# Kernel tuning notes

Hardware: AMD Instinct MI355X
Metric: run time of the kernel (lower is better)

The kernel has to match this reference:

```python
import jax, jax.numpy as jnp
import numpy as np
from jax import lax

HD = 64      # head_dim
PS = 2       # fine patch size
EPS = 1e-5   # batchnorm eps

def _conv(x, w, stride, pad, groups=1):
    return lax.conv_general_dilated(x, w, (stride, stride), ((pad, pad), (pad, pad)),
                                    feature_group_count=groups,
                                    dimension_numbers=('NCHW', 'OIHW', 'NCHW'))

def _conv_transpose(x, w, stride, pad):
    # torch ConvTranspose2d(in,out,k,stride,pad) with w [in,out,k,k]
    k = w.shape[-1]
    wt = jnp.flip(w, (2, 3)).transpose(1, 0, 2, 3)  # -> [out,in,k,k]
    e = k - 1 - pad
    return lax.conv_general_dilated(x, wt, (1, 1), ((e, e), (e, e)),
                                    lhs_dilation=(stride, stride),
                                    dimension_numbers=('NCHW', 'OIHW', 'NCHW'))

def _bn(x, g, b, m, v):
    inv = g / jnp.sqrt(v + EPS)
    return x * inv[None, :, None, None] + (b - m * inv)[None, :, None, None]

def setup_inputs() -> dict:
    key = jax.random.key(0)
    ks = jax.random.split(key, 12)
    B, C, H, W = 8, 256, 64, 64
    f = lambda k, sh, s=0.05: jax.random.normal(k, sh, jnp.float32) * s
    return {
        'x': jax.random.normal(ks[0], (B, C, H, W), jnp.float32),
        'down_w': f(ks[1], (C, C, 4, 4), 0.02), 'down_b': f(ks[2], (C,)),
        'up_w': f(ks[3], (C, C, 4, 4), 0.02), 'up_b': f(ks[4], (C,)),
        'wqkv_c': f(ks[5], (HD, 3 * HD)), 'bqkv_c': f(ks[6], (3 * HD,)),
        'wqkv_f': f(ks[7], (HD, 3 * HD)), 'bqkv_f': f(ks[8], (3 * HD,)),
        'dw_w': f(ks[9], (C, 1, 3, 3)),
        'bn1_g': jnp.ones((C,), jnp.float32), 'bn1_b': jnp.zeros((C,), jnp.float32),
        'bn1_m': jnp.zeros((C,), jnp.float32), 'bn1_v': jnp.ones((C,), jnp.float32),
        'pw_w': f(ks[10], (C, C, 1, 1)),
        'bn2_g': jnp.ones((C,), jnp.float32), 'bn2_b': jnp.zeros((C,), jnp.float32),
        'bn2_m': jnp.zeros((C,), jnp.float32), 'bn2_v': jnp.ones((C,), jnp.float32),
    }

def reference(x, down_w, down_b, up_w, up_b, wqkv_c, bqkv_c, wqkv_f, bqkv_f, dw_w,
              bn1_g, bn1_b, bn1_m, bn1_v, pw_w, bn2_g, bn2_b, bn2_m, bn2_v):
    B, C, H, W = x.shape
    nh = C // HD
    scale = HD ** -0.5

    # ---- CoarseSelfAttention: downsample -> per-head MHSA -> top-k -> upsample ----
    xd = _conv(x, down_w, 2, 1) + down_b[None, :, None, None]          # [B,C,H/2,W/2]
    h, w = H // 2, W // 2
    N = h * w
    tok = xd.reshape(B, nh, HD, N).transpose(0, 1, 3, 2)               # [B,nh,N,hd]
    q, k, v = jnp.split(tok @ wqkv_c + bqkv_c, 3, axis=-1)
    attn = jax.nn.softmax(jnp.einsum('bhnd,bhmd->bhnm', q, k) * scale, axis=-1)
    score = attn.sum(axis=-2)                                          # [B,nh,N]
    kf = max(1, N // 4)
    topk = lax.top_k(score, kf)[1]                                     # [B,nh,kf] int32
    out = jnp.einsum('bhnm,bhmd->bhnd', attn, v)
    out = out.transpose(0, 1, 3, 2).reshape(B, C, h, w)
    coarse = _conv_transpose(out, up_w, 2, 1) + up_b[None, :, None, None]  # [B,C,H,W]
    # F.interpolate to (H,W) is identity here: upsample output already matches x.

    # ---- TopkSelfAttention: gather top-k 2x2 patches, local MHSA, scatter back ----
    ph, pw = H // PS, W // PS
    xh = coarse.reshape(B, nh, HD, ph, PS, pw, PS)
    patches = xh.transpose(0, 1, 2, 3, 5, 4, 6).reshape(B, nh, HD, ph * pw, PS, PS)
    sel = jnp.take_along_axis(patches, topk[:, :, None, :, None, None], axis=3)  # [B,nh,hd,kf,PS,PS]
    tok_f = sel.reshape(B, nh, HD, kf, PS * PS).transpose(0, 1, 3, 4, 2).reshape(B, nh, kf * PS * PS, HD)
    qf, kfp, vf = jnp.split(tok_f @ wqkv_f + bqkv_f, 3, axis=-1)
    attn_f = jax.nn.softmax(jnp.einsum('bhnd,bhmd->bhnm', qf, kfp) * scale, axis=-1)
    out_f = jnp.einsum('bhnm,bhmd->bhnd', attn_f, vf)                  # [B,nh,kf*4,hd]
    out_p = out_f.reshape(B, nh, kf, PS * PS, HD).transpose(0, 1, 2, 4, 3).reshape(B, nh, kf, HD, PS, PS)
    bi = jnp.arange(B)[:, None, None]
    hi = jnp.arange(nh)[None, :, None]
    res = jnp.zeros_like(patches).at[bi, hi, :, topk].set(out_p)       # scatter (indices unique)
    region = res.reshape(B, nh, HD, ph, pw, PS, PS).transpose(0, 1, 2, 3, 5, 4, 6).reshape(B, C, H, W)

    # ---- residual + DWConv (depthwise->BN->ReLU6->pointwise->BN->ReLU6) ----
    y = coarse + region
    y = jnp.clip(_bn(_conv(y, dw_w, 1, 1, groups=C), bn1_g, bn1_b, bn1_m, bn1_v), 0.0, 6.0)
    y = jnp.clip(_bn(_conv(y, pw_w, 1, 0), bn2_g, bn2_b, bn2_m, bn2_v), 0.0, 6.0)
    return y
```

## Files before the change

kernel.cpp:

```cpp
#include <hip/hip_runtime.h>
#include <hip/hip_bf16.h>

typedef __hip_bfloat16 bf16;
typedef __bf16 bf16x8 __attribute__((ext_vector_type(8)));
typedef float f32x4 __attribute__((ext_vector_type(4)));
typedef unsigned int uintx4 __attribute__((ext_vector_type(4)));


#define OFF_XDHWC    0L
#define OFF_QH       2097152L
#define OFF_T1       0L
#define OFF_OUTC     8388608L
#define OFF_COARSE   10485760L
#define OFF_XHL      10485760L
#define OFF_PSCW     10485760L
#define OFF_SCORE    19398656L
#define OFF_TOPK     19431424L
#define OFF_DOWNW    19439616L
#define OFF_DOWNWL   19963904L
#define OFF_UPW4     20488192L
#define OFF_WQKVC    21536768L
#define OFF_BQKVC    21549056L
#define OFF_WQKVF    21549248L
#define OFF_BQKVF    21561536L
#define OFF_PWW      21561728L
#define OFF_DWW      21627264L
#define OFF_BN1S     21629568L
#define OFF_BN1T     21629824L
#define OFF_BN2S     21630080L
#define OFF_BN2T     21630336L
#define OFF_DOWNB    21630592L
#define OFF_UPB      21630848L
#define OFF_FLAG     21631104L
#define WS_FLOATS    21631360L

__device__ __forceinline__ float relu6(float v) { return v < 0.f ? 0.f : (v > 6.f ? 6.f : v); }

__device__ __forceinline__ float ldin(const void* p, long i, int flag) {
    return flag ? __bfloat162float(((const bf16*)p)[i]) : ((const float*)p)[i];
}

__device__ __forceinline__ unsigned short f2bf(float f) {
    unsigned int b = __float_as_uint(f);
    b += 0x7FFFu + ((b >> 16) & 1u);
    return (unsigned short)(b >> 16);
}

__global__ __launch_bounds__(256) void detect_kernel(const void* __restrict__ x, int* __restrict__ flag) {
    __shared__ int cnt[256];
    int tid = threadIdx.x;
    int c = 0;
    for (int i = tid; i < 4096; i += 256) {
        long idx = (long)i * 2047;
        float v = __bfloat162float(((const bf16*)x)[idx]);
        float a = fabsf(v);
        if (isfinite(v) && a > 1e-8f && a < 100.f) c++;
    }
    cnt[tid] = c; __syncthreads();
    for (int s = 128; s > 0; s >>= 1) { if (tid < s) cnt[tid] += cnt[tid + s]; __syncthreads(); }
    if (tid == 0 && cnt[0] >= 3686) *flag = 1;
}

__global__ __launch_bounds__(256) void cvt_kernel(const void* __restrict__ in, float* __restrict__ out,
                                                  int n, const int* __restrict__ flagp) {
    int flag = *flagp;
    int i = blockIdx.x * 256 + threadIdx.x;
    if (i < n) out[i] = ldin(in, i, flag);
}

__global__ __launch_bounds__(256) void cvt_bf16_kernel(const void* __restrict__ in, unsigned short* __restrict__ out,
                                                       int n, const int* __restrict__ flagp) {
    int flag = *flagp;
    int i = blockIdx.x * 256 + threadIdx.x;
    if (i < n) out[i] = f2bf(ldin(in, i, flag));
}

__global__ __launch_bounds__(256) void split_pack_kernel(const void* __restrict__ in, unsigned int* __restrict__ out,
                                                         int n, const int* __restrict__ flagp) {
    int flag = *flagp;
    int i = blockIdx.x * 256 + threadIdx.x;
    if (i < n) {
        float v = ldin(in, i, flag);
        unsigned short h = f2bf(v);
        float fh = __uint_as_float(((unsigned int)h) << 16);
        unsigned short l = f2bf(v - fh);
        out[i] = (unsigned int)h | ((unsigned int)l << 16);
    }
}

__global__ __launch_bounds__(256) void split_kernel(const void* __restrict__ in,
                                                    unsigned short* __restrict__ hi, unsigned short* __restrict__ lo,
                                                    int n, const int* __restrict__ flagp) {
    int flag = *flagp;
    int i = blockIdx.x * 256 + threadIdx.x;
    if (i < n) {
        float v = ldin(in, i, flag);
        unsigned short h = f2bf(v);
        float fh = __uint_as_float(((unsigned int)h) << 16);
        hi[i] = h;
        lo[i] = f2bf(v - fh);
    }
}

__global__ __launch_bounds__(256) void tqkv_kernel(const void* __restrict__ w, float* __restrict__ wt,
                                                   const int* __restrict__ flagp) {
    int flag = *flagp;
    int idx = blockIdx.x * 256 + threadIdx.x;
    if (idx >= 192 * 64) return;
    int j = idx >> 6, d = idx & 63;
    wt[idx] = ldin(w, d * 192 + j, flag);
}

__global__ __launch_bounds__(256) void prep_up_kernel(const void* __restrict__ w, unsigned short* __restrict__ W4,
                                                      const int* __restrict__ flagp) {
    int flag = *flagp;
    int idx = blockIdx.x * 256 + threadIdx.x;
    int cls = idx >> 18; int rem = idx & 262143;
    int co = rem >> 10; int q = rem & 1023;
    int ci = q >> 2; int j = q & 3;
    int pa = cls >> 1, pb = cls & 1;
    int jy = j >> 1, jx = j & 1;
    int ky = (pa == 0) ? (jy ? 3 : 1) : (jy ? 0 : 2);
    int kx = (pb == 0) ? (jx ? 3 : 1) : (jx ? 0 : 2);
    W4[idx] = f2bf(ldin(w, (((long)ci * 256 + co) * 4 + ky) * 4 + kx, flag));
}

__global__ void bn_prep_kernel(const void* __restrict__ g, const void* __restrict__ b,
                               const void* __restrict__ m, const void* __restrict__ v,
                               float* __restrict__ s, float* __restrict__ t,
                               const int* __restrict__ flagp) {
    int flag = *flagp;
    int c = threadIdx.x;
    float gv = ldin(g, c, flag), bv = ldin(b, c, flag);
    float mv = ldin(m, c, flag), vv = ldin(v, c, flag);
    float inv = gv / sqrtf(vv + 1e-5f);
    s[c] = inv; t[c] = bv - mv * inv;
}

__global__ __launch_bounds__(256) void gemm_mfma_x2(
    const unsigned int* __restrict__ XHL,
    const unsigned short* __restrict__ WH, const unsigned short* __restrict__ WL,
    float* __restrict__ C, const float* __restrict__ e0)
{
    __shared__ __align__(16) unsigned int Xs[40 * 68];
    __shared__ __align__(16) unsigned short Bh[64 * 72];
    __shared__ __align__(16) unsigned short Bl[64 * 72];
    int m0 = blockIdx.y * 128, n0 = blockIdx.x * 64;
    int tid = threadIdx.x;
    int w = tid >> 6, l = tid & 63, l15 = l & 15, q = l >> 4;

    int offA[11], ldsA[11];
    {
        int b = m0 >> 10;
        int iy0 = ((m0 >> 5) & 31) * 2 - 1;
        #pragma unroll
        for (int s = 0; s < 11; s++) {
            int u = s * 256 + tid;
            offA[s] = -1; ldsA[s] = -1;
            if (u < 2640) {
                int R = u / 66;
                int col = u - R * 66;
                int cl = R / 10;
                int rowl = R - cl * 10;
                ldsA[s] = R * 68 + col;
                int iy = iy0 + rowl, ix = col - 1;
                if ((unsigned)iy < 64u && (unsigned)ix < 64u)
                    offA[s] = ((b * 256 + cl) * 64 + iy) * 64 + ix;
            }
        }
    }
    unsigned int aR[11];
    uint4 bhR[2], blR[2];
    int bn = tid >> 2, bkc = (tid & 3) * 16;

    auto loadA = [&](int k0) {
        int cb = (k0 >> 4) * 4096;
        #pragma unroll
        for (int s = 0; s < 11; s++)
            aR[s] = (offA[s] >= 0) ? XHL[offA[s] + cb] : 0u;
    };
    auto storeA = [&]() {
        #pragma unroll
        for (int s = 0; s < 11; s++)
            if (ldsA[s] >= 0) Xs[ldsA[s]] = aR[s];
    };
    auto loadB = [&](int k0) {
        const unsigned short* ph = WH + (long)(n0 + bn) * 4096 + k0 + bkc;
        const unsigned short* pl = WL + (long)(n0 + bn) * 4096 + k0 + bkc;
        bhR[0] = *(const uint4*)(ph); bhR[1] = *(const uint4*)(ph + 8);
        blR[0] = *(const uint4*)(pl); blR[1] = *(const uint4*)(pl + 8);
    };
    auto storeB = [&]() {
        *(uint4*)(&Bh[bn * 72 + bkc]) = bhR[0]; *(uint4*)(&Bh[bn * 72 + bkc + 8]) = bhR[1];
        *(uint4*)(&Bl[bn * 72 + bkc]) = blR[0]; *(uint4*)(&Bl[bn * 72 + bkc + 8]) = blR[1];
    };

    f32x4 acc[2][4] = {};
    loadA(0); loadB(0);
    for (int k0 = 0; k0 < 4096; k0 += 64) {
        storeA(); storeB();
        __syncthreads();
        if (k0 + 64 < 4096) { loadA(k0 + 64); loadB(k0 + 64); }
        #pragma unroll
        for (int kk = 0; kk < 2; kk++) {
            bf16x8 bh4[4], bl4[4];
            #pragma unroll
            for (int j4 = 0; j4 < 4; j4++) {
                bh4[j4] = *(const bf16x8*)(&Bh[(j4 * 16 + l15) * 72 + kk * 32 + q * 8]);
                bl4[j4] = *(const bf16x8*)(&Bl[(j4 * 16 + l15) * 72 + kk * 32 + q * 8]);
            }
            int R0 = (kk * 2 + (q >> 1)) * 10 + 2 * w + 2 * (q & 1);
            #pragma unroll
            for (int ms = 0; ms < 2; ms++) {
                const unsigned int* rp = &Xs[R0 * 68 + 2 * (ms * 16 + l15)];
                uint2 p01 = *(const uint2*)(rp);
                uint2 p23 = *(const uint2*)(rp + 2);
                uint2 p45 = *(const uint2*)(rp + 68);
                uint2 p67 = *(const uint2*)(rp + 70);
                union { uintx4 u; bf16x8 v; } uh, ul;
                uh.u[0] = __builtin_amdgcn_perm(p01.y, p01.x, 0x05040100u);
                ul.u[0] = __builtin_amdgcn_perm(p01.y, p01.x, 0x07060302u);
                uh.u[1] = __builtin_amdgcn_perm(p23.y, p23.x, 0x05040100u);
                ul.u[1] = __builtin_amdgcn_perm(p23.y, p23.x, 0x07060302u);
                uh.u[2] = __builtin_amdgcn_perm(p45.y, p45.x, 0x05040100u);
                ul.u[2] = __builtin_amdgcn_perm(p45.y, p45.x, 0x07060302u);
                uh.u[3] = __builtin_amdgcn_perm(p67.y, p67.x, 0x05040100u);
                ul.u[3] = __builtin_amdgcn_perm(p67.y, p67.x, 0x07060302u);
                #pragma unroll
                for (int j4 = 0; j4 < 4; j4++) {
                    acc[ms][j4] = __builtin_amdgcn_mfma_f32_16x16x32_bf16(uh.v, bh4[j4], acc[ms][j4], 0, 0, 0);
                    acc[ms][j4] = __builtin_amdgcn_mfma_f32_16x16x32_bf16(uh.v, bl4[j4], acc[ms][j4], 0, 0, 0);
                    acc[ms][j4] = __builtin_amdgcn_mfma_f32_16x16x32_bf16(ul.v, bh4[j4], acc[ms][j4], 0, 0, 0);
                }
            }
        }
        __syncthreads();
    }
    #pragma unroll
    for (int ms = 0; ms < 2; ms++)
        #pragma unroll
        for (int j4 = 0; j4 < 4; j4++) {
            int n = n0 + j4 * 16 + l15;
            #pragma unroll
            for (int r = 0; r < 4; r++) {
                int m = m0 + w * 32 + ms * 16 + q * 4 + r;
                C[(long)m * 256 + n] = acc[ms][j4][r] + e0[n];
            }
        }
}

template<int EPI>
__global__ __launch_bounds__(256) void gemm_k(
    const float* __restrict__ A, const float* __restrict__ B, unsigned short* __restrict__ out,
    int K, int sAm, int sBn, const float* __restrict__ e0)
{
    __shared__ float As[16][68];
    __shared__ float Bs[16][68];
    int m0 = blockIdx.y * 64;
    int n0 = blockIdx.x * 64;
    int tid = threadIdx.x;
    int tx = tid & 15, ty = tid >> 4;
    int l4 = tid >> 2, kq = (tid & 3) * 4;
    float4 aR, bR;

    auto loadA = [&](int k0) { aR = *(const float4*)(A + (long)(m0 + l4) * sAm + (k0 + kq)); };
    auto loadB = [&](int k0) { bR = *(const float4*)(B + (long)(n0 + l4) * sBn + (k0 + kq)); };

    float acc[4][4] = {};
    loadA(0); loadB(0);
    for (int k0 = 0; k0 < K; k0 += 16) {
        As[kq + 0][l4] = aR.x; As[kq + 1][l4] = aR.y; As[kq + 2][l4] = aR.z; As[kq + 3][l4] = aR.w;
        Bs[kq + 0][l4] = bR.x; Bs[kq + 1][l4] = bR.y; Bs[kq + 2][l4] = bR.z; Bs[kq + 3][l4] = bR.w;
        __syncthreads();
        if (k0 + 16 < K) { loadA(k0 + 16); loadB(k0 + 16); }
        #pragma unroll
        for (int kk = 0; kk < 16; ++kk) {
            float4 av = *reinterpret_cast<const float4*>(&As[kk][ty * 4]);
            float4 bv = *reinterpret_cast<const float4*>(&Bs[kk][tx * 4]);
            float a[4] = {av.x, av.y, av.z, av.w};
            float b[4] = {bv.x, bv.y, bv.z, bv.w};
            #pragma unroll
            for (int i = 0; i < 4; i++)
                #pragma unroll
                for (int j = 0; j < 4; j++)
                    acc[i][j] += a[i] * b[j];
        }
        __syncthreads();
    }
    #pragma unroll
    for (int i = 0; i < 4; i++) {
        int m = m0 + ty * 4 + i;
        int bh, tok;
        if (EPI == 2) { int bi = m >> 12; int h = m & 3; tok = (m >> 2) & 1023; bh = bi * 4 + h; }
        else          { bh = m >> 10; tok = m & 1023; }
        #pragma unroll
        for (int j = 0; j < 4; j++) {
            int n = n0 + tx * 4 + j;
            float v = acc[i][j] + e0[n];
            if (n < 64) {
                v *= 0.125f;
                unsigned short hb = f2bf(v);
                float fh = __uint_as_float(((unsigned int)hb) << 16);
                unsigned short lb = f2bf(v - fh);
                long p = (((long)bh << 10) + tok) * 64 + n;
                out[p] = hb; out[p + 2097152] = lb;
            } else if (n < 128) {
                unsigned short hb = f2bf(v);
                float fh = __uint_as_float(((unsigned int)hb) << 16);
                unsigned short lb = f2bf(v - fh);
                long p = (((long)bh << 10) + tok) * 64 + (n - 64);
                out[p + 4194304] = hb; out[p + 6291456] = lb;
            } else {
                out[8388608 + (((long)bh << 6) + (n - 128)) * 1024 + tok] = f2bf(v);
            }
        }
    }
}

template<int EPI, int AMODE>
__global__ __launch_bounds__(256) void gemm_mfma(
    const float* __restrict__ A, const unsigned short* __restrict__ Bb, float* __restrict__ C,
    int K, long sAz, long sBz, int sAk, int sBn,
    const float* __restrict__ e0, const float* __restrict__ e1,
    void* __restrict__ ob, const int* __restrict__ flagp)
{
    __shared__ __align__(16) unsigned short Asb[64 * 40];
    __shared__ __align__(16) unsigned short Bsb[64 * 40];
    int z = blockIdx.z;
    if (AMODE == 0) A += (long)z * sAz;
    Bb += (long)z * sBz;
    int m0 = blockIdx.y * 64, n0 = blockIdx.x * 64;
    int tid = threadIdx.x;
    int w = tid >> 6, l = tid & 63;
    int l15 = l & 15, q = l >> 4;
    float aR[8];
    uint4 bR;

    auto loadA = [&](int k0) {
        if (AMODE == 0) {
            #pragma unroll
            for (int i = 0; i < 8; i++) {
                int idx = i * 256 + tid;
                int ml = idx & 63, kl = idx >> 6;
                aR[i] = A[(long)(k0 + kl) * sAk + (m0 + ml)];
            }
        } else {
            #pragma unroll
            for (int i = 0; i < 8; i++) {
                int idx = i * 256 + tid;
                int kl = idx & 31, ml = idx >> 5;
                int m = m0 + ml, k = k0 + kl;
                int b = m >> 10, y = (m >> 5) & 31, x2 = m & 31;
                int ci = k >> 2, j = k & 3;
                int pa = z >> 1, pb = z & 1;
                int jy = j >> 1, jx = j & 1;
                int dy = (pa == 0) ? (jy ? -1 : 0) : (jy ? 1 : 0);
                int dx = (pb == 0) ? (jx ? -1 : 0) : (jx ? 1 : 0);
                int yy = y + dy, xx = x2 + dx;
                float val = 0.f;
                if ((unsigned)yy < 32u && (unsigned)xx < 32u)
                    val = A[(((long)b * 4 + (ci >> 6)) * 1024 + yy * 32 + xx) * 64 + (ci & 63)];
                aR[i] = val;
            }
        }
    };
    auto storeA = [&]() {
        #pragma unroll
        for (int i = 0; i < 8; i++) {
            int idx = i * 256 + tid;
            int ml, kl;
            if (AMODE == 0) { ml = idx & 63; kl = idx >> 6; }
            else            { kl = idx & 31; ml = idx >> 5; }
            Asb[ml * 40 + kl] = f2bf(aR[i]);
        }
    };
    int bn = tid >> 2, bk = (tid & 3) * 8;
    auto loadB = [&](int k0) {
        bR = *(const uint4*)(Bb + (long)(n0 + bn) * sBn + (k0 + bk));
    };

    f32x4 acc[4] = {};
    loadA(0); loadB(0);
    for (int k0 = 0; k0 < K; k0 += 32) {
        storeA();
        *(uint4*)(&Bsb[bn * 40 + bk]) = bR;
        __syncthreads();
        if (k0 + 32 < K) { loadA(k0 + 32); loadB(k0 + 32); }
        bf16x8 af = *(const bf16x8*)(&Asb[(w * 16 + l15) * 40 + q * 8]);
        #pragma unroll
        for (int j4 = 0; j4 < 4; j4++) {
            bf16x8 bf = *(const bf16x8*)(&Bsb[(j4 * 16 + l15) * 40 + q * 8]);
            acc[j4] = __builtin_amdgcn_mfma_f32_16x16x32_bf16(af, bf, acc[j4], 0, 0, 0);
        }
        __syncthreads();
    }
    int oflag = (EPI == 5) ? *flagp : 0;
    #pragma unroll
    for (int j4 = 0; j4 < 4; j4++) {
        int n = n0 + j4 * 16 + l15;
        #pragma unroll
        for (int r = 0; r < 4; r++) {
            int m = m0 + w * 16 + q * 4 + r;
            float v = acc[j4][r];
            if (EPI == 4) {
                v += e0[n];
                int pa = z >> 1, pb = z & 1;
                int bi = m >> 10, y = (m >> 5) & 31, x2 = m & 31;
                C[(((long)bi * 256 + n) * 64 + (2 * y + pa)) * 64 + (2 * x2 + pb)] = v;
            } else {
                v = relu6(v * e0[n] + e1[n]);
                long oidx = (long)z * 1048576 + (long)n * 4096 + m;
                if (oflag) ((bf16*)ob)[oidx] = __float2bfloat16(v);
                else       ((float*)ob)[oidx] = v;
            }
        }
    }
}

template<bool SCORE>
__global__ __launch_bounds__(256) void attn_mfma(
    const unsigned short* __restrict__ P0,
    float* __restrict__ O, float* __restrict__ PSCW)
{
    const unsigned short* QH = P0;
    const unsigned short* QL = P0 + 2097152;
    const unsigned short* KH = P0 + 4194304;
    const unsigned short* KL = P0 + 6291456;
    const unsigned short* VT = P0 + 8388608;
    __shared__ __align__(16) unsigned short Khs[64 * 72];
    __shared__ __align__(16) unsigned short Kls[64 * 72];
    __shared__ __align__(16) unsigned short Vs[64 * 72];
    __shared__ __align__(16) unsigned short Ps[4][16 * 72];
    int bh = blockIdx.y, rt = blockIdx.x;
    int tid = threadIdx.x;
    int w = tid >> 6, l = tid & 63, l15 = l & 15, q = l >> 4;

    long qoff = (((long)bh << 10) + rt * 64 + w * 16 + l15) * 64 + q * 8;
    bf16x8 afh[2], afl[2];
    afh[0] = *(const bf16x8*)(QH + qoff);
    afh[1] = *(const bf16x8*)(QH + qoff + 32);
    afl[0] = *(const bf16x8*)(QL + qoff);
    afl[1] = *(const bf16x8*)(QL + qoff + 32);

    float mr[4], lr[4];
    #pragma unroll
    for (int r = 0; r < 4; r++) { mr[r] = -1e30f; lr[r] = 0.f; }
    f32x4 o[4] = {};

    auto stageK = [&](int t) {
        #pragma unroll
        for (int i = 0; i < 2; i++) {
            int u = tid + i * 256;
            int tok = u >> 3, dp = (u & 7) * 8;
            long g = (((long)bh << 10) + t * 64 + tok) * 64 + dp;
            *(uint4*)(Khs + tok * 72 + dp) = *(const uint4*)(KH + g);
            *(uint4*)(Kls + tok * 72 + dp) = *(const uint4*)(KL + g);
        }
    };
    auto stageV = [&](int t) {
        #pragma unroll
        for (int i = 0; i < 2; i++) {
            int u = tid + i * 256;
            int d = u >> 3, k0 = (u & 7) * 8;
            long g = (((long)bh << 6) + d) * 1024 + t * 64 + k0;
            *(uint4*)(Vs + d * 72 + k0) = *(const uint4*)(VT + g);
        }
    };
    auto computeS = [&](f32x4* s) {
        #pragma unroll
        for (int kk = 0; kk < 2; kk++)
            #pragma unroll
            for (int j4 = 0; j4 < 4; j4++) {
                bf16x8 kh8 = *(const bf16x8*)(&Khs[(j4 * 16 + l15) * 72 + kk * 32 + q * 8]);
                bf16x8 kl8 = *(const bf16x8*)(&Kls[(j4 * 16 + l15) * 72 + kk * 32 + q * 8]);
                s[j4] = __builtin_amdgcn_mfma_f32_16x16x32_bf16(afh[kk], kh8, s[j4], 0, 0, 0);
                s[j4] = __builtin_amdgcn_mfma_f32_16x16x32_bf16(afh[kk], kl8, s[j4], 0, 0, 0);
                s[j4] = __builtin_amdgcn_mfma_f32_16x16x32_bf16(afl[kk], kh8, s[j4], 0, 0, 0);
            }
    };
    auto pv = [&]() {
        #pragma unroll
        for (int kk = 0; kk < 2; kk++) {
            bf16x8 ap = *(const bf16x8*)(&Ps[w][l15 * 72 + kk * 32 + q * 8]);
            #pragma unroll
            for (int j4 = 0; j4 < 4; j4++) {
                bf16x8 bv = *(const bf16x8*)(&Vs[(j4 * 16 + l15) * 72 + kk * 32 + q * 8]);
                o[j4] = __builtin_amdgcn_mfma_f32_16x16x32_bf16(ap, bv, o[j4], 0, 0, 0);
            }
        }
    };

    if (SCORE) {
        for (int t = 0; t < 16; ++t) {
            __syncthreads();
            stageK(t);
            __syncthreads();
            f32x4 s[4] = {};
            computeS(s);
            #pragma unroll
            for (int r = 0; r < 4; r++) {
                float tm = fmaxf(fmaxf(s[0][r], s[1][r]), fmaxf(s[2][r], s[3][r]));
                #pragma unroll
                for (int off = 1; off < 16; off <<= 1) tm = fmaxf(tm, __shfl_xor(tm, off));
                float mn = fmaxf(mr[r], tm);
                float ss = __expf(s[0][r] - mn) + __expf(s[1][r] - mn)
                         + __expf(s[2][r] - mn) + __expf(s[3][r] - mn);
                #pragma unroll
                for (int off = 1; off < 16; off <<= 1) ss += __shfl_xor(ss, off);
                lr[r] = lr[r] * __expf(mr[r] - mn) + ss;
                mr[r] = mn;
            }
        }
        float linv[4];
        #pragma unroll
        for (int r = 0; r < 4; r++) linv[r] = 1.f / lr[r];
        for (int t = 0; t < 16; ++t) {
            __syncthreads();
            stageK(t); stageV(t);
            __syncthreads();
            f32x4 s[4] = {};
            computeS(s);
            float cs[4] = {0.f, 0.f, 0.f, 0.f};
            #pragma unroll
            for (int j4 = 0; j4 < 4; j4++)
                #pragma unroll
                for (int r = 0; r < 4; r++) {
                    float p = __expf(s[j4][r] - mr[r]) * linv[r];
                    cs[j4] += p;
                    Ps[w][(q * 4 + r) * 72 + j4 * 16 + l15] = f2bf(p);
                }
            #pragma unroll
            for (int j4 = 0; j4 < 4; j4++) {
                cs[j4] += __shfl_xor(cs[j4], 16);
                cs[j4] += __shfl_xor(cs[j4], 32);
            }
            if (q == 0) {
                long pb = (((long)(bh * 16 + rt) * 4 + w) << 10) + t * 64;
                #pragma unroll
                for (int j4 = 0; j4 < 4; j4++) PSCW[pb + j4 * 16 + l15] = cs[j4];
            }
            __syncthreads();
            pv();
        }
    } else {
        for (int t = 0; t < 16; ++t) {
            __syncthreads();
            stageK(t); stageV(t);
            __syncthreads();
            f32x4 s[4] = {};
            computeS(s);
            float corr[4];
            #pragma unroll
            for (int r = 0; r < 4; r++) {
                float tm = fmaxf(fmaxf(s[0][r], s[1][r]), fmaxf(s[2][r], s[3][r]));
                #pragma unroll
                for (int off = 1; off < 16; off <<= 1) tm = fmaxf(tm, __shfl_xor(tm, off));
                float mn = fmaxf(mr[r], tm);
                corr[r] = __expf(mr[r] - mn);
                mr[r] = mn;
            }
            float ssr[4] = {0.f, 0.f, 0.f, 0.f};
            #pragma unroll
            for (int j4 = 0; j4 < 4; j4++)
                #pragma unroll
                for (int r = 0; r < 4; r++) {
                    float p = __expf(s[j4][r] - mr[r]);
                    ssr[r] += p;
                    Ps[w][(q * 4 + r) * 72 + j4 * 16 + l15] = f2bf(p);
                }
            #pragma unroll
            for (int r = 0; r < 4; r++) {
                float ss = ssr[r];
                #pragma unroll
                for (int off = 1; off < 16; off <<= 1) ss += __shfl_xor(ss, off);
                lr[r] = lr[r] * corr[r] + ss;
            }
            #pragma unroll
            for (int j4 = 0; j4 < 4; j4++)
                #pragma unroll
                for (int r = 0; r < 4; r++) o[j4][r] *= corr[r];
            __syncthreads();
            pv();
        }
    }

    float fin[4];
    #pragma unroll
    for (int r = 0; r < 4; r++) fin[r] = SCORE ? 1.f : (1.f / lr[r]);
    long obase = (((long)bh << 10) + rt * 64 + w * 16 + q * 4) * 64;
    #pragma unroll
    for (int j4 = 0; j4 < 4; j4++)
        #pragma unroll
        for (int r = 0; r < 4; r++)
            O[obase + (long)r * 64 + j4 * 16 + l15] = o[j4][r] * fin[r];
}

__global__ __launch_bounds__(256) void score_reduce_kernel(const float* __restrict__ PSCW, float* __restrict__ score) {
    int idx = blockIdx.x * 256 + threadIdx.x;
    int bh = idx >> 10, c = idx & 1023;
    float s = 0.f;
    for (int rw = 0; rw < 64; rw++) s += PSCW[(((long)bh * 64 + rw) << 10) + c];
    score[idx] = s;
}

__global__ __launch_bounds__(256) void topk_kernel(const float* __restrict__ score, int* __restrict__ topk) {
    __shared__ float s[1024];
    int z = blockIdx.x; int tid = threadIdx.x;
    for (int i = tid; i < 1024; i += 256) {
        float v = score[z * 1024 + i];
        s[i] = (v == v) ? v : -INFINITY;
    }
    __syncthreads();
    for (int i = tid; i < 1024; i += 256) {
        float si = s[i]; int r = 0;
        for (int j = 0; j < 1024; j++) {
            float sj = s[j];
            r += (sj > si) || (sj == si && j < i);
        }
        if (r < 256) topk[z * 256 + r] = i;
    }
}

__global__ __launch_bounds__(256) void gather_tokf_kernel(const float* __restrict__ coarse,
                                                          const int* __restrict__ topk,
                                                          float* __restrict__ tokf) {
    long idx = (long)blockIdx.x * 256 + threadIdx.x;
    int d = (int)(idx & 63); int t = (int)((idx >> 6) & 3);
    int j = (int)((idx >> 8) & 255); int bh = (int)(idx >> 16);
    int p = topk[bh * 256 + j] & 1023;
    int py = p >> 5, px = p & 31;
    int dy = t >> 1, dx = t & 1;
    int b = bh >> 2, h = bh & 3;
    tokf[idx] = coarse[(((long)b * 256 + h * 64 + d) * 64 + (2 * py + dy)) * 64 + (2 * px + dx)];
}

__global__ __launch_bounds__(256) void scatter_add_kernel(float* __restrict__ coarse,
                                                          const int* __restrict__ topk,
                                                          const float* __restrict__ outf) {
    long idx = (long)blockIdx.x * 256 + threadIdx.x;
    int d = (int)(idx & 63); int t = (int)((idx >> 6) & 3);
    int j = (int)((idx >> 8) & 255); int bh = (int)(idx >> 16);
    int p = topk[bh * 256 + j] & 1023;
    int py = p >> 5, px = p & 31;
    int dy = t >> 1, dx = t & 1;
    int b = bh >> 2, h = bh & 3;
    coarse[(((long)b * 256 + h * 64 + d) * 64 + (2 * py + dy)) * 64 + (2 * px + dx)] += outf[idx];
}

__global__ __launch_bounds__(64) void dw_bn_relu6_kernel(const float* __restrict__ y, const float* __restrict__ w9,
                                                         const float* __restrict__ s1, const float* __restrict__ t1,
                                                         float* __restrict__ out) {
    int gid = blockIdx.x;
    int row = gid & 63; int bc = gid >> 6; int c = bc & 255;
    int x = threadIdx.x;
    const float* base = y + (long)bc * 4096;
    float acc = 0.f;
    #pragma unroll
    for (int ky = 0; ky < 3; ky++) {
        int yy = row + ky - 1;
        if (yy < 0 || yy >= 64) continue;
        #pragma unroll
        for (int kx = 0; kx < 3; kx++) {
            int xx = x + kx - 1;
            if (xx < 0 || xx >= 64) continue;
            acc += base[yy * 64 + xx] * w9[c * 9 + ky * 3 + kx];
        }
    }
    out[(long)gid * 64 + x] = relu6(acc * s1[c] + t1[c]);
}

extern "C" void kernel_launch(void* const* d_in, const int* in_sizes, int n_in,
                              void* d_out, int out_size, void* d_ws, size_t ws_size,
                              hipStream_t stream) {
    if (ws_size < (size_t)WS_FLOATS * 4) return;

    const void* x      = d_in[0];
    const void* down_w = d_in[1];
    const void* down_b = d_in[2];
    const void* up_w   = d_in[3];
    const void* up_b   = d_in[4];
    const void* wqkv_c = d_in[5];
    const void* bqkv_c = d_in[6];
    const void* wqkv_f = d_in[7];
    const void* bqkv_f = d_in[8];
    const void* dw_w   = d_in[9];
    const void* bn1_g  = d_in[10];
    const void* bn1_b  = d_in[11];
    const void* bn1_m  = d_in[12];
    const void* bn1_v  = d_in[13];
    const void* pw_w   = d_in[14];
    const void* bn2_g  = d_in[15];
    const void* bn2_b  = d_in[16];
    const void* bn2_m  = d_in[17];
    const void* bn2_v  = d_in[18];

    float* ws = (float*)d_ws;
    int* flagp = (int*)(ws + OFF_FLAG);
    dim3 blk(256);

    hipMemsetAsync(flagp, 0, sizeof(int), stream);
    detect_kernel<<<1, blk, 0, stream>>>(x, flagp);

    split_pack_kernel<<<32768, blk, 0, stream>>>(x, (unsigned int*)(ws + OFF_XHL), 8388608, flagp);
    split_kernel<<<4096, blk, 0, stream>>>(down_w, (unsigned short*)(ws + OFF_DOWNW),
                                           (unsigned short*)(ws + OFF_DOWNWL), 1048576, flagp);
    cvt_kernel<<<1, blk, 0, stream>>>(down_b, ws + OFF_DOWNB, 256, flagp);
    cvt_kernel<<<1, blk, 0, stream>>>(up_b, ws + OFF_UPB, 256, flagp);
    cvt_kernel<<<1, blk, 0, stream>>>(bqkv_c, ws + OFF_BQKVC, 192, flagp);
    cvt_kernel<<<1, blk, 0, stream>>>(bqkv_f, ws + OFF_BQKVF, 192, flagp);
    cvt_bf16_kernel<<<256, blk, 0, stream>>>(pw_w, (unsigned short*)(ws + OFF_PWW), 65536, flagp);
    cvt_kernel<<<9, blk, 0, stream>>>(dw_w, ws + OFF_DWW, 2304, flagp);
    tqkv_kernel<<<48, blk, 0, stream>>>(wqkv_c, ws + OFF_WQKVC, flagp);
    tqkv_kernel<<<48, blk, 0, stream>>>(wqkv_f, ws + OFF_WQKVF, flagp);
    prep_up_kernel<<<4096, blk, 0, stream>>>(up_w, (unsigned short*)(ws + OFF_UPW4), flagp);
    bn_prep_kernel<<<1, blk, 0, stream>>>(bn1_g, bn1_b, bn1_m, bn1_v, ws + OFF_BN1S, ws + OFF_BN1T, flagp);
    bn_prep_kernel<<<1, blk, 0, stream>>>(bn2_g, bn2_b, bn2_m, bn2_v, ws + OFF_BN2S, ws + OFF_BN2T, flagp);

    gemm_mfma_x2<<<dim3(4, 64, 1), blk, 0, stream>>>((const unsigned int*)(ws + OFF_XHL),
        (const unsigned short*)(ws + OFF_DOWNW), (const unsigned short*)(ws + OFF_DOWNWL),
        ws + OFF_XDHWC, ws + OFF_DOWNB);

    gemm_k<2><<<dim3(3, 512, 1), blk, 0, stream>>>(ws + OFF_XDHWC, ws + OFF_WQKVC,
        (unsigned short*)(ws + OFF_QH), 64, 64, 64, ws + OFF_BQKVC);

    attn_mfma<true><<<dim3(16, 32), blk, 0, stream>>>((const unsigned short*)(ws + OFF_QH),
        ws + OFF_OUTC, ws + OFF_PSCW);
    score_reduce_kernel<<<128, blk, 0, stream>>>(ws + OFF_PSCW, ws + OFF_SCORE);
    topk_kernel<<<32, blk, 0, stream>>>(ws + OFF_SCORE, (int*)(ws + OFF_TOPK));

    gemm_mfma<4, 2><<<dim3(4, 128, 4), blk, 0, stream>>>(ws + OFF_OUTC, (unsigned short*)(ws + OFF_UPW4),
        ws + OFF_COARSE, 1024, 0, 262144, 0, 1024, ws + OFF_UPB, nullptr, nullptr, flagp);

    gather_tokf_kernel<<<8192, blk, 0, stream>>>(ws + OFF_COARSE, (const int*)(ws + OFF_TOPK), ws + OFF_XDHWC);
    gemm_k<3><<<dim3(3, 512, 1), blk, 0, stream>>>(ws + OFF_XDHWC, ws + OFF_WQKVF,
        (unsigned short*)(ws + OFF_QH), 64, 64, 64, ws + OFF_BQKVF);
    attn_mfma<false><<<dim3(16, 32), blk, 0, stream>>>((const unsigned short*)(ws + OFF_QH),
        ws + OFF_OUTC, nullptr);
    scatter_add_kernel<<<8192, blk, 0, stream>>>(ws + OFF_COARSE, (const int*)(ws + OFF_TOPK), ws + OFF_OUTC);

    dw_bn_relu6_kernel<<<131072, dim3(64), 0, stream>>>(ws + OFF_COARSE, ws + OFF_DWW,
        ws + OFF_BN1S, ws + OFF_BN1T, ws + OFF_T1);

    gemm_mfma<5, 0><<<dim3(4, 64, 8), blk, 0, stream>>>(ws + OFF_T1, (unsigned short*)(ws + OFF_PWW),
        nullptr, 256, 1048576, 0, 4096, 256, ws + OFF_BN2S, ws + OFF_BN2T, d_out, flagp);
}
```

Before: 850.7 us.

## Split-K and smaller M tile for downsample conv GEMM, sum partials in QKV GEMM

The downsample conv GEMM now uses 64-row M tiles and splits K into two halves across blockIdx.z. This raises the grid from 256 to 1024 blocks to improve occupancy across the CUs. The two partial results go to separate buffers, and the following QKV GEMM adds them while loading its A operand, so no separate reduction pass is needed. The cost is extra global traffic for the second partial buffer and less reuse of each B tile within a block.

After: 839.5 us. No clear change (-1.3%).

```diff
diff --git a/kernel.cpp b/kernel.cpp
--- a/kernel.cpp
+++ b/kernel.cpp
@@ -140,28 +140,29 @@
 __global__ __launch_bounds__(256) void gemm_mfma_x2(
     const unsigned int* __restrict__ XHL,
     const unsigned short* __restrict__ WH, const unsigned short* __restrict__ WL,
-    float* __restrict__ C, const float* __restrict__ e0)
+    float* __restrict__ C0, float* __restrict__ C1, const float* __restrict__ e0)
 {
-    __shared__ __align__(16) unsigned int Xs[40 * 68];
+    __shared__ __align__(16) unsigned int Xs[24 * 68];
     __shared__ __align__(16) unsigned short Bh[64 * 72];
     __shared__ __align__(16) unsigned short Bl[64 * 72];
-    int m0 = blockIdx.y * 128, n0 = blockIdx.x * 64;
+    int m0 = blockIdx.y * 64, n0 = blockIdx.x * 64;
+    int kz = blockIdx.z * 2048;
     int tid = threadIdx.x;
     int w = tid >> 6, l = tid & 63, l15 = l & 15, q = l >> 4;
 
-    int offA[11], ldsA[11];
+    int offA[7], ldsA[7];
     {
         int b = m0 >> 10;
         int iy0 = ((m0 >> 5) & 31) * 2 - 1;
         #pragma unroll
-        for (int s = 0; s < 11; s++) {
+        for (int s = 0; s < 7; s++) {
             int u = s * 256 + tid;
             offA[s] = -1; ldsA[s] = -1;
-            if (u < 2640) {
+            if (u < 1584) {
                 int R = u / 66;
                 int col = u - R * 66;
-                int cl = R / 10;
-                int rowl = R - cl * 10;
+                int cl = R / 6;
+                int rowl = R - cl * 6;
                 ldsA[s] = R * 68 + col;
                 int iy = iy0 + rowl, ix = col - 1;
                 if ((unsigned)iy < 64u && (unsigned)ix < 64u)
@@ -169,24 +170,24 @@
             }
         }
     }
-    unsigned int aR[11];
+    unsigned int aR[7];
     uint4 bhR[2], blR[2];
     int bn = tid >> 2, bkc = (tid & 3) * 16;
 
     auto loadA = [&](int k0) {
-        int cb = (k0 >> 4) * 4096;
-        #pragma unroll
-        for (int s = 0; s < 11; s++)
+        int cb = (((kz + k0) >> 4)) * 4096;
+        #pragma unroll
+        for (int s = 0; s < 7; s++)
             aR[s] = (offA[s] >= 0) ? XHL[offA[s] + cb] : 0u;
     };
     auto storeA = [&]() {
         #pragma unroll
-        for (int s = 0; s < 11; s++)
+        for (int s = 0; s < 7; s++)
             if (ldsA[s] >= 0) Xs[ldsA[s]] = aR[s];
     };
     auto loadB = [&](int k0) {
-        const unsigned short* ph = WH + (long)(n0 + bn) * 4096 + k0 + bkc;
-        const unsigned short* pl = WL + (long)(n0 + bn) * 4096 + k0 + bkc;
+        const unsigned short* ph = WH + (long)(n0 + bn) * 4096 + kz + k0 + bkc;
+        const unsigned short* pl = WL + (long)(n0 + bn) * 4096 + kz + k0 + bkc;
         bhR[0] = *(const uint4*)(ph); bhR[1] = *(const uint4*)(ph + 8);
         blR[0] = *(const uint4*)(pl); blR[1] = *(const uint4*)(pl + 8);
     };
@@ -195,12 +196,12 @@
         *(uint4*)(&Bl[bn * 72 + bkc]) = blR[0]; *(uint4*)(&Bl[bn * 72 + bkc + 8]) = blR[1];
     };
 
-    f32x4 acc[2][4] = {};
+    f32x4 acc[4] = {};
     loadA(0); loadB(0);
-    for (int k0 = 0; k0 < 4096; k0 += 64) {
+    for (int k0 = 0; k0 < 2048; k0 += 64) {
         storeA(); storeB();
         __syncthreads();
-        if (k0 + 64 < 4096) { loadA(k0 + 64); loadB(k0 + 64); }
+        if (k0 + 64 < 2048) { loadA(k0 + 64); loadB(k0 + 64); }
         #pragma unroll
         for (int kk = 0; kk < 2; kk++) {
             bf16x8 bh4[4], bl4[4];
@@ -209,50 +210,47 @@
                 bh4[j4] = *(const bf16x8*)(&Bh[(j4 * 16 + l15) * 72 + kk * 32 + q * 8]);
                 bl4[j4] = *(const bf16x8*)(&Bl[(j4 * 16 + l15) * 72 + kk * 32 + q * 8]);
             }
-            int R0 = (kk * 2 + (q >> 1)) * 10 + 2 * w + 2 * (q & 1);
-            #pragma unroll
-            for (int ms = 0; ms < 2; ms++) {
-                const unsigned int* rp = &Xs[R0 * 68 + 2 * (ms * 16 + l15)];
-                uint2 p01 = *(const uint2*)(rp);
-                uint2 p23 = *(const uint2*)(rp + 2);
-                uint2 p45 = *(const uint2*)(rp + 68);
-                uint2 p67 = *(const uint2*)(rp + 70);
-                union { uintx4 u; bf16x8 v; } uh, ul;
-                uh.u[0] = __builtin_amdgcn_perm(p01.y, p01.x, 0x05040100u);
-                ul.u[0] = __builtin_amdgcn_perm(p01.y, p01.x, 0x07060302u);
-                uh.u[1] = __builtin_amdgcn_perm(p23.y, p23.x, 0x05040100u);
-                ul.u[1] = __builtin_amdgcn_perm(p23.y, p23.x, 0x07060302u);
-                uh.u[2] = __builtin_amdgcn_perm(p45.y, p45.x, 0x05040100u);
-                ul.u[2] = __builtin_amdgcn_perm(p45.y, p45.x, 0x07060302u);
-                uh.u[3] = __builtin_amdgcn_perm(p67.y, p67.x, 0x05040100u);
-                ul.u[3] = __builtin_amdgcn_perm(p67.y, p67.x, 0x07060302u);
-                #pragma unroll
-                for (int j4 = 0; j4 < 4; j4++) {
-                    acc[ms][j4] = __builtin_amdgcn_mfma_f32_16x16x32_bf16(uh.v, bh4[j4], acc[ms][j4], 0, 0, 0);
-                    acc[ms][j4] = __builtin_amdgcn_mfma_f32_16x16x32_bf16(uh.v, bl4[j4], acc[ms][j4], 0, 0, 0);
-                    acc[ms][j4] = __builtin_amdgcn_mfma_f32_16x16x32_bf16(ul.v, bh4[j4], acc[ms][j4], 0, 0, 0);
-                }
+            int R0 = (2 * kk + (q >> 1)) * 6 + 2 * (w >> 1) + 2 * (q & 1);
+            const unsigned int* rp = &Xs[R0 * 68 + 2 * ((w & 1) * 16 + l15)];
+            uint2 p01 = *(const uint2*)(rp);
+            uint2 p23 = *(const uint2*)(rp + 2);
+            uint2 p45 = *(const uint2*)(rp + 68);
+            uint2 p67 = *(const uint2*)(rp + 70);
+            union { uintx4 u; bf16x8 v; } uh, ul;
+            uh.u[0] = __builtin_amdgcn_perm(p01.y, p01.x, 0x05040100u);
+            ul.u[0] = __builtin_amdgcn_perm(p01.y, p01.x, 0x07060302u);
+            uh.u[1] = __builtin_amdgcn_perm(p23.y, p23.x, 0x05040100u);
+            ul.u[1] = __builtin_amdgcn_perm(p23.y, p23.x, 0x07060302u);
+            uh.u[2] = __builtin_amdgcn_perm(p45.y, p45.x, 0x05040100u);
+            ul.u[2] = __builtin_amdgcn_perm(p45.y, p45.x, 0x07060302u);
+            uh.u[3] = __builtin_amdgcn_perm(p67.y, p67.x, 0x05040100u);
+            ul.u[3] = __builtin_amdgcn_perm(p67.y, p67.x, 0x07060302u);
+            #pragma unroll
+            for (int j4 = 0; j4 < 4; j4++) {
+                acc[j4] = __builtin_amdgcn_mfma_f32_16x16x32_bf16(uh.v, bh4[j4], acc[j4], 0, 0, 0);
+                acc[j4] = __builtin_amdgcn_mfma_f32_16x16x32_bf16(uh.v, bl4[j4], acc[j4], 0, 0, 0);
+                acc[j4] = __builtin_amdgcn_mfma_f32_16x16x32_bf16(ul.v, bh4[j4], acc[j4], 0, 0, 0);
             }
         }
         __syncthreads();
     }
+    float* Cz = blockIdx.z ? C1 : C0;
     #pragma unroll
-    for (int ms = 0; ms < 2; ms++)
-        #pragma unroll
-        for (int j4 = 0; j4 < 4; j4++) {
-            int n = n0 + j4 * 16 + l15;
-            #pragma unroll
-            for (int r = 0; r < 4; r++) {
-                int m = m0 + w * 32 + ms * 16 + q * 4 + r;
-                C[(long)m * 256 + n] = acc[ms][j4][r] + e0[n];
-            }
-        }
-}
-
-template<int EPI>
+    for (int j4 = 0; j4 < 4; j4++) {
+        int n = n0 + j4 * 16 + l15;
+        float bias = blockIdx.z ? 0.f : e0[n];
+        #pragma unroll
+        for (int r = 0; r < 4; r++) {
+            int m = m0 + w * 16 + q * 4 + r;
+            Cz[(long)m * 256 + n] = acc[j4][r] + bias;
+        }
+    }
+}
+
+template<int EPI, bool SUM2>
 __global__ __launch_bounds__(256) void gemm_k(
-    const float* __restrict__ A, const float* __restrict__ B, unsigned short* __restrict__ out,
-    int K, int sAm, int sBn, const float* __restrict__ e0)
+    const float* __restrict__ A, const float* __restrict__ A2, const float* __restrict__ B,
+    unsigned short* __restrict__ out, int K, int sAm, int sBn, const float* __restrict__ e0)
 {
     __shared__ float As[16][68];
     __shared__ float Bs[16][68];
@@ -263,7 +261,14 @@
     int l4 = tid >> 2, kq = (tid & 3) * 4;
     float4 aR, bR;
 
-    auto loadA = [&](int k0) { aR = *(const float4*)(A + (long)(m0 + l4) * sAm + (k0 + kq)); };
+    auto loadA = [&](int k0) {
+        long off = (long)(m0 + l4) * sAm + (k0 + kq);
+        aR = *(const float4*)(A + off);
+        if (SUM2) {
+            float4 a2 = *(const float4*)(A2 + off);
+            aR.x += a2.x; aR.y += a2.y; aR.z += a2.z; aR.w += a2.w;
+        }
+    };
     auto loadB = [&](int k0) { bR = *(const float4*)(B + (long)(n0 + l4) * sBn + (k0 + kq)); };
 
     float acc[4][4] = {};
@@ -716,11 +721,11 @@
     bn_prep_kernel<<<1, blk, 0, stream>>>(bn1_g, bn1_b, bn1_m, bn1_v, ws + OFF_BN1S, ws + OFF_BN1T, flagp);
     bn_prep_kernel<<<1, blk, 0, stream>>>(bn2_g, bn2_b, bn2_m, bn2_v, ws + OFF_BN2S, ws + OFF_BN2T, flagp);
 
-    gemm_mfma_x2<<<dim3(4, 64, 1), blk, 0, stream>>>((const unsigned int*)(ws + OFF_XHL),
+    gemm_mfma_x2<<<dim3(4, 128, 2), blk, 0, stream>>>((const unsigned int*)(ws + OFF_XHL),
         (const unsigned short*)(ws + OFF_DOWNW), (const unsigned short*)(ws + OFF_DOWNWL),
-        ws + OFF_XDHWC, ws + OFF_DOWNB);
-
-    gemm_k<2><<<dim3(3, 512, 1), blk, 0, stream>>>(ws + OFF_XDHWC, ws + OFF_WQKVC,
+        ws + OFF_XDHWC, ws + OFF_OUTC, ws + OFF_DOWNB);
+
+    gemm_k<2, true><<<dim3(3, 512, 1), blk, 0, stream>>>(ws + OFF_XDHWC, ws + OFF_OUTC, ws + OFF_WQKVC,
         (unsigned short*)(ws + OFF_QH), 64, 64, 64, ws + OFF_BQKVC);
 
     attn_mfma<true><<<dim3(16, 32), blk, 0, stream>>>((const unsigned short*)(ws + OFF_QH),
@@ -732,7 +737,7 @@
         ws + OFF_COARSE, 1024, 0, 262144, 0, 1024, ws + OFF_UPB, nullptr, nullptr, flagp);
 
     gather_tokf_kernel<<<8192, blk, 0, stream>>>(ws + OFF_COARSE, (const int*)(ws + OFF_TOPK), ws + OFF_XDHWC);
-    gemm_k<3><<<dim3(3, 512, 1), blk, 0, stream>>>(ws + OFF_XDHWC, ws + OFF_WQKVF,
+    gemm_k<3, false><<<dim3(3, 512, 1), blk, 0, stream>>>(ws + OFF_XDHWC, nullptr, ws + OFF_WQKVF,
         (unsigned short*)(ws + OFF_QH), 64, 64, 64, ws + OFF_BQKVF);
     attn_mfma<false><<<dim3(16, 32), blk, 0, stream>>>((const unsigned short*)(ws + OFF_QH),
         ws + OFF_OUTC, nullptr);
```
